# Performance work log

Measured on AMD Instinct MI355X. Metric: run time of the kernel, lower is better.

The kernel has to match this reference:

```python
import jax, jax.numpy as jnp
import numpy as np

IN_CH = 256
HID = 32
OUT_CH = 32
EPS = 1e-5


def setup_inputs() -> dict:
    key = jax.random.key(0)
    ks = jax.random.split(key, 7)
    B, L = 1, 256
    x = jax.random.normal(ks[0], (B, L, IN_CH), dtype=jnp.float32)
    # nn.Linear(in_channels, hidden_dim)
    W1 = jax.random.normal(ks[1], (IN_CH, HID), dtype=jnp.float32) / np.sqrt(IN_CH)
    b1 = jnp.zeros((HID,), dtype=jnp.float32)
    # nn.LayerNorm(hidden_dim * hidden_dim)
    gamma = jnp.ones((HID * HID,), dtype=jnp.float32)
    beta = jnp.zeros((HID * HID,), dtype=jnp.float32)
    # nn.Linear(hidden_dim * hidden_dim, out_channels)
    W2 = jax.random.normal(ks[2], (HID * HID, OUT_CH), dtype=jnp.float32) / np.sqrt(HID * HID)
    b2 = jnp.zeros((OUT_CH,), dtype=jnp.float32)
    return {"x": x, "W1": W1, "b1": b1, "gamma": gamma, "beta": beta, "W2": W2, "b2": b2}


def reference(x, W1, b1, gamma, beta, W2, b2):
    # a: [B, L, HID]
    a = jnp.einsum('bic,ch->bih', x, W1) + b1
    # outer product: [B, I, J, D, E] -> flatten to [B, I, J, D*E]
    outer = jnp.einsum('bid,bje->bijde', a, a)
    B, I, J, D, E = outer.shape
    outer = outer.reshape(B, I, J, D * E)
    # LayerNorm over last dim
    mu = jnp.mean(outer, axis=-1, keepdims=True)
    var = jnp.mean(jnp.square(outer - mu), axis=-1, keepdims=True)
    normed = (outer - mu) * jax.lax.rsqrt(var + EPS) * gamma + beta
    # final projection: [B, I, J, OUT_CH]
    return jnp.einsum('bijk,ko->bijo', normed, W2) + b2
```

## Files before the change

### kernel.cpp

```cpp
#include <hip/hip_runtime.h>

#define LSEQ 256
#define INC  256
#define HID  32
#define OUTC 32
#define DE   1024
#define EPSV 1e-5f

#define ASTR 260
#define TSTR 36

__global__ __launch_bounds__(256) void k1_a_stats(
    const float* __restrict__ x, const float* __restrict__ W1, const float* __restrict__ b1,
    const float* __restrict__ gamma, const float* __restrict__ beta,
    const float* __restrict__ W2, const float* __restrict__ b2,
    float* __restrict__ a, float* __restrict__ S, float* __restrict__ Q,
    float* __restrict__ GW, float* __restrict__ C)
{
    __shared__ float sh0[256];
    __shared__ float sh1[256];
    __shared__ float shA[128];
    __shared__ float shB[128];
    const int t = threadIdx.x;
    const int b = blockIdx.x;
    if (b < 64) {
        const int r = t >> 6;
        const int h = (t >> 5) & 1;
        const int d = t & 31;
        const int i = b * 4 + r;
        const float* xr = x + i * INC + h * 128;
        const float* w  = W1 + (h * 128) * HID + d;
        float p0 = 0.f, p1 = 0.f;
        #pragma unroll 8
        for (int k = 0; k < 64; ++k) {
            p0 = fmaf(xr[2 * k],     w[(2 * k) * HID],     p0);
            p1 = fmaf(xr[2 * k + 1], w[(2 * k + 1) * HID], p1);
        }
        sh0[t] = p0 + p1;
        __syncthreads();
        if (h == 0) {
            const float tot = sh0[t] + sh0[t + 32] + b1[d];
            a[i * HID + d] = tot;
            shA[r * 32 + d] = tot;
            shB[r * 32 + d] = tot * tot;
        }
        __syncthreads();
        if (t < 4) {
            float s = 0.f, q = 0.f;
            #pragma unroll
            for (int d2 = 0; d2 < 32; ++d2) { s += shA[t * 32 + d2]; q += shB[t * 32 + d2]; }
            S[b * 4 + t] = s;
            Q[b * 4 + t] = q;
        }
    } else {
        const int o = t & 31, chunk = t >> 5;
        float gw = 0.f, bw = 0.f;
        for (int k = 0; k < 128; ++k) {
            const int de = chunk * 128 + k;
            const float w = W2[de * OUTC + o];
            gw = fmaf(gamma[de], w, gw);
            bw = fmaf(beta[de],  w, bw);
        }
        sh0[t] = gw; sh1[t] = bw;
        __syncthreads();
        if (t < 32) {
            float g = 0.f, bb = 0.f;
            #pragma unroll
            for (int c2 = 0; c2 < 8; ++c2) { g += sh0[c2 * 32 + t]; bb += sh1[c2 * 32 + t]; }
            GW[t] = g;
            C[t]  = bb + b2[t];
        }
    }
}

__global__ __launch_bounds__(256) void k2_fused(
    const float* __restrict__ a, const float* __restrict__ S, const float* __restrict__ Q,
    const float* __restrict__ GW, const float* __restrict__ C,
    const float* __restrict__ gamma, const float* __restrict__ W2,
    float* __restrict__ out)
{
    const int j = blockIdx.x, t = threadIdx.x;
    __shared__ float aPad[32 * ASTR];
    __shared__ float tPad[32 * TSTR];
    __shared__ float gL[DE];
    __shared__ float sL[LSEQ];
    __shared__ float qL[LSEQ];
    __shared__ float gwL[OUTC], cL[OUTC];

    {
        const float4* ar4 = (const float4*)(a + t * HID);
        const int base = (t >> 3) * ASTR + (t & 7);
        #pragma unroll
        for (int c = 0; c < 8; ++c) {
            const float4 v = ar4[c];
            const int d = c * 4;
            aPad[base + (d + 0) * 8] = v.x;
            aPad[base + (d + 1) * 8] = v.y;
            aPad[base + (d + 2) * 8] = v.z;
            aPad[base + (d + 3) * 8] = v.w;
        }
    }
    #pragma unroll
    for (int k = t; k < DE; k += 256) gL[k] = gamma[k];
    sL[t] = S[t];
    qL[t] = Q[t];
    if (t < OUTC) { gwL[t] = GW[t]; cL[t] = C[t]; }
    __syncthreads();

    {
        const int d = t >> 3, o0 = (t & 7) * 4;
        const int jb = (j >> 3) * ASTR + (j & 7);
        float4 acc = {0.f, 0.f, 0.f, 0.f};
        #pragma unroll
        for (int e = 0; e < 32; ++e) {
            const float g = gL[d * 32 + e] * aPad[jb + e * 8];
            const float4 w = *(const float4*)(W2 + (d * 32 + e) * OUTC + o0);
            acc.x = fmaf(g, w.x, acc.x);
            acc.y = fmaf(g, w.y, acc.y);
            acc.z = fmaf(g, w.z, acc.z);
            acc.w = fmaf(g, w.w, acc.w);
        }
        *(float4*)(tPad + d * TSTR + o0) = acc;
    }
    __syncthreads();

    const int iT = t >> 3, oT = t & 7;
    const int abase = iT * ASTR;
    float acc[8][4];
    #pragma unroll
    for (int m = 0; m < 8; ++m)
        #pragma unroll
        for (int k = 0; k < 4; ++k) acc[m][k] = 0.f;

    #pragma unroll
    for (int d = 0; d < 32; ++d) {
        const float4 a0 = *(const float4*)(aPad + abase + d * 8);
        const float4 a1 = *(const float4*)(aPad + abase + d * 8 + 4);
        const float4 tf = *(const float4*)(tPad + d * TSTR + oT * 4);
        const float am[8] = {a0.x, a0.y, a0.z, a0.w, a1.x, a1.y, a1.z, a1.w};
        const float tk[4] = {tf.x, tf.y, tf.z, tf.w};
        #pragma unroll
        for (int m = 0; m < 8; ++m)
            #pragma unroll
            for (int k = 0; k < 4; ++k)
                acc[m][k] = fmaf(am[m], tk[k], acc[m][k]);
    }

    const float Sj = sL[j], Qj = qL[j];
    const float gw0 = gwL[oT * 4 + 0], gw1 = gwL[oT * 4 + 1];
    const float gw2 = gwL[oT * 4 + 2], gw3 = gwL[oT * 4 + 3];
    const float c0 = cL[oT * 4 + 0], c1 = cL[oT * 4 + 1];
    const float c2 = cL[oT * 4 + 2], c3 = cL[oT * 4 + 3];

    #pragma unroll
    for (int m = 0; m < 8; ++m) {
        const int i = iT * 8 + m;
        const float Si = sL[i], Qi = qL[i];
        const float mu  = Si * Sj * (1.0f / 1024.0f);
        const float ex2 = Qi * Qj * (1.0f / 1024.0f);
        const float var = ex2 - mu * mu;
        const float r   = rsqrtf(var + EPSV);
        float4 o4;
        o4.x = fmaf(r, acc[m][0] - mu * gw0, c0);
        o4.y = fmaf(r, acc[m][1] - mu * gw1, c1);
        o4.z = fmaf(r, acc[m][2] - mu * gw2, c2);
        o4.w = fmaf(r, acc[m][3] - mu * gw3, c3);
        *(float4*)(out + (i * LSEQ + j) * OUTC + oT * 4) = o4;
    }
}

extern "C" void kernel_launch(void* const* d_in, const int* in_sizes, int n_in,
                              void* d_out, int out_size, void* d_ws, size_t ws_size,
                              hipStream_t stream)
{
    const float* x     = (const float*)d_in[0];
    const float* W1    = (const float*)d_in[1];
    const float* b1    = (const float*)d_in[2];
    const float* gamma = (const float*)d_in[3];
    const float* beta  = (const float*)d_in[4];
    const float* W2    = (const float*)d_in[5];
    const float* b2    = (const float*)d_in[6];
    float* out = (float*)d_out;

    float* ws = (float*)d_ws;
    float* a  = ws;
    float* S  = ws + 8192;
    float* Q  = ws + 8448;
    float* GW = ws + 8704;
    float* C  = ws + 8736;

    k1_a_stats<<<65, 256, 0, stream>>>(x, W1, b1, gamma, beta, W2, b2, a, S, Q, GW, C);
    k2_fused<<<LSEQ, 256, 0, stream>>>(a, S, Q, GW, C, gamma, W2, out);
}
```

Before: 82.21 us.

## Precompute per-j T matrix in first kernel and split output GEMM across 512 blocks

The per-j T = (gamma*a_j)·W2 projection moves from the output kernel into the first kernel, which now runs one block per sequence row and writes T to workspace. The second kernel then only loads T and half of the a rows, computing 128 output rows per block across 512 blocks instead of 256. This removes redundant gamma loading and a sync from the output kernel and doubles its block count for better occupancy. The cost is an extra 1MB workspace write and read of T, and more first-kernel blocks.

```diff
diff --git a/kernel.cpp b/kernel.cpp
--- a/kernel.cpp
+++ b/kernel.cpp
@@ -7,51 +7,67 @@
 #define DE   1024
 #define EPSV 1e-5f
 
-#define ASTR 260
+#define ASTR 264
 #define TSTR 36
 
-__global__ __launch_bounds__(256) void k1_a_stats(
+__global__ __launch_bounds__(256) void k1_aT(
     const float* __restrict__ x, const float* __restrict__ W1, const float* __restrict__ b1,
     const float* __restrict__ gamma, const float* __restrict__ beta,
     const float* __restrict__ W2, const float* __restrict__ b2,
     float* __restrict__ a, float* __restrict__ S, float* __restrict__ Q,
-    float* __restrict__ GW, float* __restrict__ C)
+    float* __restrict__ T, float* __restrict__ GW, float* __restrict__ C)
 {
-    __shared__ float sh0[256];
-    __shared__ float sh1[256];
-    __shared__ float shA[128];
-    __shared__ float shB[128];
+    __shared__ float sh[256];
+    __shared__ float sh2[256];
+    __shared__ float xL[256];
+    __shared__ float aL[32];
     const int t = threadIdx.x;
     const int b = blockIdx.x;
-    if (b < 64) {
-        const int r = t >> 6;
-        const int h = (t >> 5) & 1;
-        const int d = t & 31;
-        const int i = b * 4 + r;
-        const float* xr = x + i * INC + h * 128;
-        const float* w  = W1 + (h * 128) * HID + d;
+
+    if (b < 256) {
+        const int j = b;
+        xL[t] = x[j * INC + t];
+        __syncthreads();
+
+        const int d = t & 31, kc = t >> 5;
+        const float* w = W1 + (kc * 32) * HID + d;
         float p0 = 0.f, p1 = 0.f;
-        #pragma unroll 8
-        for (int k = 0; k < 64; ++k) {
-            p0 = fmaf(xr[2 * k],     w[(2 * k) * HID],     p0);
-            p1 = fmaf(xr[2 * k + 1], w[(2 * k + 1) * HID], p1);
+        #pragma unroll
+        for (int k = 0; k < 16; ++k) {
+            p0 = fmaf(xL[kc * 32 + 2 * k],     w[(2 * k) * HID],     p0);
+            p1 = fmaf(xL[kc * 32 + 2 * k + 1], w[(2 * k + 1) * HID], p1);
         }
-        sh0[t] = p0 + p1;
+        sh[t] = p0 + p1;
         __syncthreads();
-        if (h == 0) {
-            const float tot = sh0[t] + sh0[t + 32] + b1[d];
-            a[i * HID + d] = tot;
-            shA[r * 32 + d] = tot;
-            shB[r * 32 + d] = tot * tot;
+
+        if (t < 32) {
+            float tot = b1[t];
+            #pragma unroll
+            for (int c = 0; c < 8; ++c) tot += sh[c * 32 + t];
+            aL[t] = tot;
+            a[j * HID + t] = tot;
+            float s = tot, q = tot * tot;
+            #pragma unroll
+            for (int off = 16; off > 0; off >>= 1) {
+                s += __shfl_xor(s, off);
+                q += __shfl_xor(q, off);
+            }
+            if (t == 0) { S[j] = s; Q[j] = q; }
         }
         __syncthreads();
-        if (t < 4) {
-            float s = 0.f, q = 0.f;
-            #pragma unroll
-            for (int d2 = 0; d2 < 32; ++d2) { s += shA[t * 32 + d2]; q += shB[t * 32 + d2]; }
-            S[b * 4 + t] = s;
-            Q[b * 4 + t] = q;
+
+        const int dd = t >> 3, o4 = (t & 7) * 4;
+        float4 acc = {0.f, 0.f, 0.f, 0.f};
+        #pragma unroll
+        for (int e = 0; e < 32; ++e) {
+            const float g = gamma[dd * 32 + e] * aL[e];
+            const float4 wv = *(const float4*)(W2 + (dd * 32 + e) * OUTC + o4);
+            acc.x = fmaf(g, wv.x, acc.x);
+            acc.y = fmaf(g, wv.y, acc.y);
+            acc.z = fmaf(g, wv.z, acc.z);
+            acc.w = fmaf(g, wv.w, acc.w);
         }
+        *(float4*)(T + j * DE + dd * 32 + o4) = acc;
     } else {
         const int o = t & 31, chunk = t >> 5;
         float gw = 0.f, bw = 0.f;
@@ -61,86 +77,72 @@
             gw = fmaf(gamma[de], w, gw);
             bw = fmaf(beta[de],  w, bw);
         }
-        sh0[t] = gw; sh1[t] = bw;
+        sh[t] = gw; sh2[t] = bw;
         __syncthreads();
         if (t < 32) {
             float g = 0.f, bb = 0.f;
             #pragma unroll
-            for (int c2 = 0; c2 < 8; ++c2) { g += sh0[c2 * 32 + t]; bb += sh1[c2 * 32 + t]; }
+            for (int c2 = 0; c2 < 8; ++c2) { g += sh[c2 * 32 + t]; bb += sh2[c2 * 32 + t]; }
             GW[t] = g;
             C[t]  = bb + b2[t];
         }
     }
 }
 
-__global__ __launch_bounds__(256) void k2_fused(
+__global__ __launch_bounds__(256) void k2_gemm(
     const float* __restrict__ a, const float* __restrict__ S, const float* __restrict__ Q,
     const float* __restrict__ GW, const float* __restrict__ C,
-    const float* __restrict__ gamma, const float* __restrict__ W2,
-    float* __restrict__ out)
+    const float* __restrict__ T, float* __restrict__ out)
 {
-    const int j = blockIdx.x, t = threadIdx.x;
-    __shared__ float aPad[32 * ASTR];
+    const int bid = blockIdx.x;
+    const int j = bid & 255, half = bid >> 8;
+    const int t = threadIdx.x;
+    __shared__ float aPad[16 * ASTR];
     __shared__ float tPad[32 * TSTR];
-    __shared__ float gL[DE];
     __shared__ float sL[LSEQ];
     __shared__ float qL[LSEQ];
     __shared__ float gwL[OUTC], cL[OUTC];
 
     {
-        const float4* ar4 = (const float4*)(a + t * HID);
-        const int base = (t >> 3) * ASTR + (t & 7);
+        const int r = t >> 1, p = t & 1;
+        const float4* ar4 = (const float4*)(a + (half * 128 + r) * HID + p * 16);
+        const int base = (r >> 3) * ASTR + (r & 7);
         #pragma unroll
-        for (int c = 0; c < 8; ++c) {
+        for (int c = 0; c < 4; ++c) {
             const float4 v = ar4[c];
-            const int d = c * 4;
-            aPad[base + (d + 0) * 8] = v.x;
-            aPad[base + (d + 1) * 8] = v.y;
-            aPad[base + (d + 2) * 8] = v.z;
-            aPad[base + (d + 3) * 8] = v.w;
+            const int dd = p * 16 + c * 4;
+            aPad[base + (dd + 0) * 8] = v.x;
+            aPad[base + (dd + 1) * 8] = v.y;
+            aPad[base + (dd + 2) * 8] = v.z;
+            aPad[base + (dd + 3) * 8] = v.w;
         }
     }
-    #pragma unroll
-    for (int k = t; k < DE; k += 256) gL[k] = gamma[k];
+    {
+        const float4 v = *(const float4*)(T + j * DE + t * 4);
+        const int dd = t >> 3, o4 = (t & 7) * 4;
+        *(float4*)(tPad + dd * TSTR + o4) = v;
+    }
     sL[t] = S[t];
     qL[t] = Q[t];
     if (t < OUTC) { gwL[t] = GW[t]; cL[t] = C[t]; }
     __syncthreads();
 
-    {
-        const int d = t >> 3, o0 = (t & 7) * 4;
-        const int jb = (j >> 3) * ASTR + (j & 7);
-        float4 acc = {0.f, 0.f, 0.f, 0.f};
-        #pragma unroll
-        for (int e = 0; e < 32; ++e) {
-            const float g = gL[d * 32 + e] * aPad[jb + e * 8];
-            const float4 w = *(const float4*)(W2 + (d * 32 + e) * OUTC + o0);
-            acc.x = fmaf(g, w.x, acc.x);
-            acc.y = fmaf(g, w.y, acc.y);
-            acc.z = fmaf(g, w.z, acc.z);
-            acc.w = fmaf(g, w.w, acc.w);
-        }
-        *(float4*)(tPad + d * TSTR + o0) = acc;
-    }
-    __syncthreads();
-
     const int iT = t >> 3, oT = t & 7;
-    const int abase = iT * ASTR;
-    float acc[8][4];
+    const int abase = (iT >> 1) * ASTR + (iT & 1) * 4;
+    float acc[4][4];
     #pragma unroll
-    for (int m = 0; m < 8; ++m)
+    for (int m = 0; m < 4; ++m)
         #pragma unroll
         for (int k = 0; k < 4; ++k) acc[m][k] = 0.f;
 
     #pragma unroll
     for (int d = 0; d < 32; ++d) {
-        const float4 a0 = *(const float4*)(aPad + abase + d * 8);
-        const float4 a1 = *(const float4*)(aPad + abase + d * 8 + 4);
-        const float4 tf = *(const float4*)(tPad + d * TSTR + oT * 4);
-        const float am[8] = {a0.x, a0.y, a0.z, a0.w, a1.x, a1.y, a1.z, a1.w};
-        const float tk[4] = {tf.x, tf.y, tf.z, tf.w};
+        const float4 av = *(const float4*)(aPad + abase + d * 8);
+        const float4 tv = *(const float4*)(tPad + d * TSTR + oT * 4);
+        const float am[4] = {av.x, av.y, av.z, av.w};
+        const float tk[4] = {tv.x, tv.y, tv.z, tv.w};
         #pragma unroll
-        for (int m = 0; m < 8; ++m)
+        for (int m = 0; m < 4; ++m)
             #pragma unroll
             for (int k = 0; k < 4; ++k)
                 acc[m][k] = fmaf(am[m], tk[k], acc[m][k]);
@@ -153,19 +155,20 @@
     const float c2 = cL[oT * 4 + 2], c3 = cL[oT * 4 + 3];
 
     #pragma unroll
-    for (int m = 0; m < 8; ++m) {
-        const int i = iT * 8 + m;
+    for (int m = 0; m < 4; ++m) {
+        const int lr = (iT >> 1) * 8 + (iT & 1) * 4 + m;
+        const int i = half * 128 + lr;
         const float Si = sL[i], Qi = qL[i];
         const float mu  = Si * Sj * (1.0f / 1024.0f);
         const float ex2 = Qi * Qj * (1.0f / 1024.0f);
         const float var = ex2 - mu * mu;
         const float r   = rsqrtf(var + EPSV);
-        float4 o4;
-        o4.x = fmaf(r, acc[m][0] - mu * gw0, c0);
-        o4.y = fmaf(r, acc[m][1] - mu * gw1, c1);
-        o4.z = fmaf(r, acc[m][2] - mu * gw2, c2);
-        o4.w = fmaf(r, acc[m][3] - mu * gw3, c3);
-        *(float4*)(out + (i * LSEQ + j) * OUTC + oT * 4) = o4;
+        float4 o4v;
+        o4v.x = fmaf(r, acc[m][0] - mu * gw0, c0);
+        o4v.y = fmaf(r, acc[m][1] - mu * gw1, c1);
+        o4v.z = fmaf(r, acc[m][2] - mu * gw2, c2);
+        o4v.w = fmaf(r, acc[m][3] - mu * gw3, c3);
+        *(float4*)(out + (i * LSEQ + j) * OUTC + oT * 4) = o4v;
     }
 }
 
@@ -188,7 +191,8 @@
     float* Q  = ws + 8448;
     float* GW = ws + 8704;
     float* C  = ws + 8736;
+    float* T  = ws + 8768;
 
-    k1_a_stats<<<65, 256, 0, stream>>>(x, W1, b1, gamma, beta, W2, b2, a, S, Q, GW, C);
-    k2_fused<<<LSEQ, 256, 0, stream>>>(a, S, Q, GW, C, gamma, W2, out);
+    k1_aT<<<257, 256, 0, stream>>>(x, W1, b1, gamma, beta, W2, b2, a, S, Q, T, GW, C);
+    k2_gemm<<<512, 256, 0, stream>>>(a, S, Q, GW, C, T, out);
 }
```

After: 77.57 us, median of 2. 1.06x faster.
